# Kernel optimization log

Measured on AMD Instinct MI355X. Metric: run time of the kernel, lower is better.

## Reference

```python
import jax, jax.numpy as jnp
import numpy as np

B, N, D, H = 32, 1024, 512, 8
DH = D // H


def setup_inputs() -> dict:
    key = jax.random.key(0)
    ks = jax.random.split(key, 7)
    s = 1.0 / np.sqrt(D)
    return {
        "x": jax.random.normal(ks[0], (B, N, D), dtype=jnp.float32),
        "Wq": jax.random.uniform(ks[1], (D, D), jnp.float32, -s, s),
        "bq": jax.random.uniform(ks[2], (D,), jnp.float32, -s, s),
        "Wk": jax.random.uniform(ks[3], (D, D), jnp.float32, -s, s),
        "bk": jax.random.uniform(ks[4], (D,), jnp.float32, -s, s),
        "Wv": jax.random.uniform(ks[5], (D, D), jnp.float32, -s, s),
        "bv": jax.random.uniform(ks[6], (D,), jnp.float32, -s, s),
    }


def reference(x, Wq, bq, Wk, bk, Wv, bv):
    # Linear projections (torch Linear: y = x @ W.T + b)
    q = x @ Wq.T + bq
    k = x @ Wk.T + bk
    v = x @ Wv.T + bv
    # Faithful to the original: RAW reshape [B,N,D] -> [B,H,N,D/H] (no transpose!)
    q = q.reshape(B, H, N, DH)
    k = k.reshape(B, H, N, DH)
    v = v.reshape(B, H, N, DH)
    # Scaled dot-product attention
    scores = jnp.einsum("bhnd,bhmd->bhnm", q, k) / jnp.sqrt(jnp.float32(DH))
    attn = jax.nn.softmax(scores, axis=-1)
    y = jnp.einsum("bhnm,bhmd->bhnd", attn, v)
    # Faithful to the original: raw reshape [B,H,N,DH] -> [B,N,H*DH]
    return y.reshape(B, N, H * DH)
```

## Files before the change

kernel.cpp:

```cpp
#include <hip/hip_runtime.h>
#include <hip/hip_bf16.h>
#include <stdint.h>

#define AS_G __attribute__((address_space(1)))
#define AS_L __attribute__((address_space(3)))

typedef short bf16x8 __attribute__((ext_vector_type(8)));
typedef float f32x4  __attribute__((ext_vector_type(4)));
typedef float f32x16 __attribute__((ext_vector_type(16)));
typedef unsigned int u32x2 __attribute__((ext_vector_type(2)));

constexpr int   M_ROWS = 32768;
constexpr float QSCALE = 0.18033688011112042f;

__device__ __forceinline__ ushort f2bf(float f) {
  union { __hip_bfloat16 h; ushort u; } c;
  c.h = __float2bfloat16(f);
  return c.u;
}
__device__ __forceinline__ uint32_t pack2bf(float lo, float hi) {
  union { __hip_bfloat162 b; uint32_t u; } r;
  r.b.x = __float2bfloat16(lo);
  r.b.y = __float2bfloat16(hi);
  return r.u;
}
__device__ __forceinline__ u32x2 pswap(uint32_t x) {
  return __builtin_amdgcn_permlane32_swap(x, x, false, false);
}
__device__ __forceinline__ void gload16(const ushort* g, ushort* l) {
  __builtin_amdgcn_global_load_lds((const AS_G uint32_t*)g, (AS_L uint32_t*)l, 16, 0, 0);
}

__device__ __forceinline__ void cvt8(const float* __restrict__ in,
                                     ushort* __restrict__ out, int i) {
  float4 a = reinterpret_cast<const float4*>(in)[2 * i];
  float4 b = reinterpret_cast<const float4*>(in)[2 * i + 1];
  ushort4 o0 = {f2bf(a.x), f2bf(a.y), f2bf(a.z), f2bf(a.w)};
  ushort4 o1 = {f2bf(b.x), f2bf(b.y), f2bf(b.z), f2bf(b.w)};
  reinterpret_cast<ushort4*>(out)[2 * i]     = o0;
  reinterpret_cast<ushort4*>(out)[2 * i + 1] = o1;
}

__global__ __launch_bounds__(256) void cvt_all_kernel(
    const float* __restrict__ x,  const float* __restrict__ wq,
    const float* __restrict__ wk, const float* __restrict__ wv,
    ushort* __restrict__ xb, ushort* __restrict__ wb) {
  const int b = blockIdx.x, t = threadIdx.x;
  if (b < 2048) {
    const int i0 = b * 256 + t;
#pragma unroll
    for (int rep = 0; rep < 4; ++rep) cvt8(x, xb, i0 + rep * 524288);
  } else {
    const int c = b - 2048, m = c >> 7;
    const float* src = (m == 0) ? wq : (m == 1 ? wk : wv);
    cvt8(src, wb + m * 262144, (c & 127) * 256 + t);
  }
}

__global__ __launch_bounds__(256) void qkv_gemm_kernel(
    const ushort* __restrict__ Xb, const ushort* __restrict__ Wall,
    const float* __restrict__ bq, const float* __restrict__ bk,
    const float* __restrict__ bv,
    ushort* __restrict__ QKV)
{
  __shared__ ushort As[128 * 64];
  __shared__ ushort Bs[128 * 64];

  const int tile = blockIdx.x;
  const int mt  = tile & 255;
  const int cz  = tile >> 8;
  const int mat = cz >> 2;
  const int nt  = cz & 3;

  const ushort* W    = Wall + (size_t)mat * (512 * 512);
  const float*  bias = (mat == 0) ? bq : (mat == 1 ? bk : bv);
  ushort*       Out  = QKV + (size_t)mat * ((size_t)M_ROWS * 512);
  const float   oscale = (mat == 0) ? QSCALE : 1.0f;

  const int m0 = mt * 128, n0 = nt * 128;
  const int t = threadIdx.x, lane = t & 63, wave = t >> 6;
  const int wr = wave >> 1, wc = wave & 1;
  const int l15 = lane & 15, lg = lane >> 4;

  f32x4 acc[4][4];
#pragma unroll
  for (int i = 0; i < 4; i++)
#pragma unroll
    for (int j = 0; j < 4; j++) acc[i][j] = {0.f, 0.f, 0.f, 0.f};

  for (int kt = 0; kt < 8; ++kt) {
    const int k0 = kt * 64;
    __syncthreads();
#pragma unroll
    for (int i = 0; i < 4; ++i) {
      int c = i * 256 + t, row = c >> 3, col8 = (c & 7) * 8;
      gload16(Xb + (size_t)(m0 + row) * 512 + k0 + col8, As + c * 8);
    }
#pragma unroll
    for (int i = 0; i < 4; ++i) {
      int c = i * 256 + t, row = c >> 3, col8 = (c & 7) * 8;
      gload16(W + (size_t)(n0 + row) * 512 + k0 + col8, Bs + c * 8);
    }
    __syncthreads();
#pragma unroll
    for (int ks = 0; ks < 2; ++ks) {
      bf16x8 af[4], bfr[4];
#pragma unroll
      for (int i = 0; i < 4; ++i) {
        af[i]  = *(const bf16x8*)(As + (wr * 64 + i * 16 + l15) * 64 + ks * 32 + lg * 8);
        bfr[i] = *(const bf16x8*)(Bs + (wc * 64 + i * 16 + l15) * 64 + ks * 32 + lg * 8);
      }
#pragma unroll
      for (int i = 0; i < 4; ++i)
#pragma unroll
        for (int j = 0; j < 4; ++j)
          acc[i][j] = __builtin_amdgcn_mfma_f32_16x16x32_bf16(af[i], bfr[j], acc[i][j], 0, 0, 0);
    }
  }
#pragma unroll
  for (int j = 0; j < 4; ++j) {
    const int col = n0 + wc * 64 + j * 16 + l15;
    const float bc = bias[col];
#pragma unroll
    for (int i = 0; i < 4; ++i) {
      const int row0 = m0 + wr * 64 + i * 16 + lg * 4;
#pragma unroll
      for (int r = 0; r < 4; ++r)
        Out[(size_t)(row0 + r) * 512 + col] = f2bf((acc[i][j][r] + bc) * oscale);
    }
  }
}

__global__ __launch_bounds__(256) void vtrans_kernel(
    const ushort* __restrict__ Vn, ushort* __restrict__ VT)
{
  __shared__ ushort T[64][258];
  const int bh = blockIdx.x >> 2, nc = blockIdx.x & 3;
  const ushort* src = Vn + (size_t)bh * 65536 + nc * 16384;
  ushort* dst = VT + (size_t)bh * 65536 + nc * 256;
  const int t = threadIdx.x;
#pragma unroll
  for (int i = 0; i < 8; ++i) {
    int c = i * 256 + t, n = c >> 3, col8 = (c & 7) * 8;
    ushort tmp[8];
    *(int4*)tmp = *(const int4*)(src + n * 64 + col8);
#pragma unroll
    for (int j = 0; j < 8; ++j) T[col8 + j][n] = tmp[j];
  }
  __syncthreads();
#pragma unroll
  for (int i = 0; i < 8; ++i) {
    int c = i * 256 + t, dh = c >> 5, a8 = (c & 31) * 8;
    const int w = a8 & 63;
    const int pbase = (a8 & 192) + (w >> 5) * 32 + ((w >> 4) & 1) * 16
                    + ((w >> 3) & 1) * 4;
    ushort tmp[8];
    *(uint64_t*)(tmp)     = *(const uint64_t*)(&T[dh][pbase]);
    *(uint64_t*)(tmp + 4) = *(const uint64_t*)(&T[dh][pbase + 8]);
    *(int4*)(dst + (size_t)dh * 1024 + a8) = *(const int4*)tmp;
  }
}

__global__ __launch_bounds__(256, 4) void attn_kernel(
    const ushort* __restrict__ QKV,
    const ushort* __restrict__ VTg_,
    float* __restrict__ Out)
{
  constexpr int PLANE = M_ROWS * 512;
  __shared__ ushort SMEM[64 * 258];
  ushort* sK = SMEM;
  ushort* sV = SMEM + 8192;
  float* Lbuf = (float*)SMEM;

  const int raw = blockIdx.x;
  const int blk = ((raw & 7) << 8) | (raw >> 3);
  const int bh = blk >> 3, qb = blk & 7;
  const ushort* Qg  = QKV + (size_t)bh * 65536;
  const ushort* Kg  = QKV + (size_t)PLANE + (size_t)bh * 65536;
  const ushort* Vtg = VTg_ + (size_t)bh * 65536;

  const int t = threadIdx.x, lane = t & 63, wave = t >> 6;
  const int l31 = lane & 31, h = lane >> 5;
  const int q = qb * 128 + wave * 32 + l31;

  bf16x8 qf[4];
#pragma unroll
  for (int ks = 0; ks < 4; ++ks)
    qf[ks] = *(const bf16x8*)(Qg + (size_t)q * 64 + ks * 16 + h * 8);

  float mrow = -1e30f, lrow = 0.f;
  f32x16 o[2];
#pragma unroll
  for (int r = 0; r < 16; ++r) { o[0][r] = 0.f; o[1][r] = 0.f; }

#pragma unroll
  for (int i = 0; i < 2; ++i) {
    int c = i * 256 + t, row = c >> 3, slot = c & 7;
    gload16(Kg + (size_t)row * 64 + ((slot ^ (row & 7)) << 3), sK + c * 8);
    gload16(Vtg + (size_t)row * 1024 + ((slot ^ (row & 7)) << 3), sV + c * 8);
  }
  __syncthreads();

  for (int kv = 0; kv < 16; ++kv) {
    const int cur = kv & 1;
    if (kv < 15) {
      const int nx = cur ^ 1, kn = kv + 1;
#pragma unroll
      for (int i = 0; i < 2; ++i) {
        int c = i * 256 + t, row = c >> 3, slot = c & 7;
        gload16(Kg + (size_t)(kn * 64 + row) * 64 + ((slot ^ (row & 7)) << 3),
                sK + nx * 4096 + c * 8);
        gload16(Vtg + (size_t)row * 1024 + kn * 64 + ((slot ^ (row & 7)) << 3),
                sV + nx * 4096 + c * 8);
      }
    }
    const ushort* Kc = sK + cur * 4096;
    const ushort* Vc = sV + cur * 4096;

    f32x16 st[2];
#pragma unroll
    for (int tt = 0; tt < 2; ++tt) {
      f32x16 a;
#pragma unroll
      for (int r = 0; r < 16; ++r) a[r] = 0.f;
      __builtin_amdgcn_s_setprio(1);
#pragma unroll
      for (int ks = 0; ks < 4; ++ks) {
        const int krow = tt * 32 + l31;
        bf16x8 kf = *(const bf16x8*)(Kc + krow * 64 + (((ks * 2 + h) ^ (krow & 7)) << 3));
        a = __builtin_amdgcn_mfma_f32_32x32x16_bf16(kf, qf[ks], a, 0, 0, 0);
      }
      __builtin_amdgcn_s_setprio(0);
      st[tt] = a;
    }

    float mx;
    {
      float t8[8];
#pragma unroll
      for (int i = 0; i < 8; ++i)
        t8[i] = fmaxf(fmaxf(st[0][i], st[0][i + 8]), fmaxf(st[1][i], st[1][i + 8]));
      float a0 = fmaxf(fmaxf(t8[0], t8[1]), fmaxf(t8[2], t8[3]));
      float a1 = fmaxf(fmaxf(t8[4], t8[5]), fmaxf(t8[6], t8[7]));
      mx = fmaxf(a0, a1);
    }
    {
      u32x2 d = pswap(__float_as_uint(mx));
      mx = fmaxf(__uint_as_float(d.x), __uint_as_float(d.y));
    }
    if (!__all(mx - mrow <= 8.0f)) {
      const float mnew = fmaxf(mrow, mx);
      const float alpha = exp2f(mrow - mnew);
      mrow = mnew;
      lrow *= alpha;
#pragma unroll
      for (int r = 0; r < 16; ++r) { o[0][r] *= alpha; o[1][r] *= alpha; }
    }
#pragma unroll
    for (int tt = 0; tt < 2; ++tt)
#pragma unroll
      for (int r = 0; r < 16; ++r) st[tt][r] = exp2f(st[tt][r] - mrow);
    {
      float s8[8];
#pragma unroll
      for (int i = 0; i < 8; ++i)
        s8[i] = (st[0][i] + st[0][i + 8]) + (st[1][i] + st[1][i + 8]);
      float rs = ((s8[0] + s8[1]) + (s8[2] + s8[3]))
               + ((s8[4] + s8[5]) + (s8[6] + s8[7]));
      u32x2 d = pswap(__float_as_uint(rs));
      lrow += __uint_as_float(d.x) + __uint_as_float(d.y);
    }

#pragma unroll
    for (int tt = 0; tt < 2; ++tt) {
#pragma unroll
      for (int s = 0; s < 2; ++s) {
        union { uint32_t u[4]; bf16x8 v; } pf;
#pragma unroll
        for (int i = 0; i < 4; ++i)
          pf.u[i] = pack2bf(st[tt][8 * s + 2 * i], st[tt][8 * s + 2 * i + 1]);
        const int ks2 = tt * 2 + s;
        __builtin_amdgcn_s_setprio(1);
#pragma unroll
        for (int dt = 0; dt < 2; ++dt) {
          const int drow = dt * 32 + l31;
          bf16x8 vf = *(const bf16x8*)(Vc + drow * 64 +
                                       (((ks2 * 2 + h) ^ (drow & 7)) << 3));
          o[dt] = __builtin_amdgcn_mfma_f32_32x32x16_bf16(vf, pf.v, o[dt], 0, 0, 0);
        }
        __builtin_amdgcn_s_setprio(0);
      }
    }
    __syncthreads();
  }

  const float linv = 1.f / lrow;
#pragma unroll
  for (int dt = 0; dt < 2; ++dt)
#pragma unroll
    for (int r = 0; r < 16; ++r) {
      const int d = dt * 32 + (r & 3) + 8 * (r >> 2) + 4 * h;
      Lbuf[d * 129 + wave * 32 + l31] = o[dt][r] * linv;
    }
  __syncthreads();
  {
    const int qloc = t >> 1, dh = (t & 1) * 32;
    float* ob = Out + (size_t)bh * 65536 + (size_t)(qb * 128 + qloc) * 64 + dh;
#pragma unroll
    for (int c = 0; c < 8; ++c) {
      float4 v = { Lbuf[(dh + 4 * c + 0) * 129 + qloc],
                   Lbuf[(dh + 4 * c + 1) * 129 + qloc],
                   Lbuf[(dh + 4 * c + 2) * 129 + qloc],
                   Lbuf[(dh + 4 * c + 3) * 129 + qloc] };
      *(float4*)(ob + 4 * c) = v;
    }
  }
}

extern "C" void kernel_launch(void* const* d_in, const int* in_sizes, int n_in,
                              void* d_out, int out_size, void* d_ws, size_t ws_size,
                              hipStream_t stream) {
  (void)in_sizes; (void)n_in; (void)out_size; (void)ws_size;
  const float* x  = (const float*)d_in[0];
  const float* Wq = (const float*)d_in[1];
  const float* bq = (const float*)d_in[2];
  const float* Wk = (const float*)d_in[3];
  const float* bk = (const float*)d_in[4];
  const float* Wv = (const float*)d_in[5];
  const float* bv = (const float*)d_in[6];

  ushort* Xb  = (ushort*)d_ws;
  ushort* VT  = (ushort*)d_ws;
  ushort* Wb  = (ushort*)((char*)d_ws + 33554432);
  ushort* QKV = (ushort*)((char*)d_ws + 35127296);
  ushort* Vn  = QKV + 2 * (size_t)M_ROWS * 512;

  cvt_all_kernel<<<2432, 256, 0, stream>>>(x, Wq, Wk, Wv, Xb, Wb);

  qkv_gemm_kernel<<<256 * 12, 256, 0, stream>>>(Xb, Wb, bq, bk, bv, QKV);

  vtrans_kernel<<<1024, 256, 0, stream>>>(Vn, VT);

  attn_kernel<<<256 * 8, 256, 0, stream>>>(QKV, VT, (float*)d_out);
}
```

Measured before the change: 235.6 us.

## Read V directly from global memory and shrink LDS to raise occupancy

Stops staging the transposed V tiles in LDS and has each lane load its V fragments straight from global memory inside the PV MFMA loop. The epilogue transpose buffer is cut to a 32x129 float array, with the output written in two halves, and launch bounds rise from 4 to 6 blocks per SIMD. The aim is to let more workgroups fit per CU and hide latency better, at the cost of uncoalesced per-lane global loads of V in the inner loop, which depend on L2 hits.

After: 529.1 us. 2.25x slower.

```diff
diff --git a/kernel.cpp b/kernel.cpp
--- a/kernel.cpp
+++ b/kernel.cpp
@@ -161,16 +161,14 @@
   }
 }
 
-__global__ __launch_bounds__(256, 4) void attn_kernel(
+__global__ __launch_bounds__(256, 6) void attn_kernel(
     const ushort* __restrict__ QKV,
     const ushort* __restrict__ VTg_,
     float* __restrict__ Out)
 {
   constexpr int PLANE = M_ROWS * 512;
-  __shared__ ushort SMEM[64 * 258];
-  ushort* sK = SMEM;
-  ushort* sV = SMEM + 8192;
-  float* Lbuf = (float*)SMEM;
+  __shared__ float Lbuf[32 * 129];
+  ushort* sK = (ushort*)Lbuf;
 
   const int raw = blockIdx.x;
   const int blk = ((raw & 7) << 8) | (raw >> 3);
@@ -197,7 +195,6 @@
   for (int i = 0; i < 2; ++i) {
     int c = i * 256 + t, row = c >> 3, slot = c & 7;
     gload16(Kg + (size_t)row * 64 + ((slot ^ (row & 7)) << 3), sK + c * 8);
-    gload16(Vtg + (size_t)row * 1024 + ((slot ^ (row & 7)) << 3), sV + c * 8);
   }
   __syncthreads();
 
@@ -210,12 +207,10 @@
         int c = i * 256 + t, row = c >> 3, slot = c & 7;
         gload16(Kg + (size_t)(kn * 64 + row) * 64 + ((slot ^ (row & 7)) << 3),
                 sK + nx * 4096 + c * 8);
-        gload16(Vtg + (size_t)row * 1024 + kn * 64 + ((slot ^ (row & 7)) << 3),
-                sV + nx * 4096 + c * 8);
       }
     }
-    const ushort* Kc = sK + cur * 4096;
-    const ushort* Vc = sV + cur * 4096;
+    const ushort* Kc  = sK + cur * 4096;
+    const ushort* Vkv = Vtg + kv * 64;
 
     f32x16 st[2];
 #pragma unroll
@@ -284,8 +279,7 @@
 #pragma unroll
         for (int dt = 0; dt < 2; ++dt) {
           const int drow = dt * 32 + l31;
-          bf16x8 vf = *(const bf16x8*)(Vc + drow * 64 +
-                                       (((ks2 * 2 + h) ^ (drow & 7)) << 3));
+          bf16x8 vf = *(const bf16x8*)(Vkv + (size_t)drow * 1024 + ks2 * 16 + h * 8);
           o[dt] = __builtin_amdgcn_mfma_f32_32x32x16_bf16(vf, pf.v, o[dt], 0, 0, 0);
         }
         __builtin_amdgcn_s_setprio(0);
@@ -296,22 +290,23 @@
 
   const float linv = 1.f / lrow;
 #pragma unroll
-  for (int dt = 0; dt < 2; ++dt)
+  for (int half = 0; half < 2; ++half) {
+    __syncthreads();
 #pragma unroll
     for (int r = 0; r < 16; ++r) {
-      const int d = dt * 32 + (r & 3) + 8 * (r >> 2) + 4 * h;
-      Lbuf[d * 129 + wave * 32 + l31] = o[dt][r] * linv;
-    }
-  __syncthreads();
-  {
-    const int qloc = t >> 1, dh = (t & 1) * 32;
-    float* ob = Out + (size_t)bh * 65536 + (size_t)(qb * 128 + qloc) * 64 + dh;
-#pragma unroll
-    for (int c = 0; c < 8; ++c) {
-      float4 v = { Lbuf[(dh + 4 * c + 0) * 129 + qloc],
-                   Lbuf[(dh + 4 * c + 1) * 129 + qloc],
-                   Lbuf[(dh + 4 * c + 2) * 129 + qloc],
-                   Lbuf[(dh + 4 * c + 3) * 129 + qloc] };
+      const int dloc = (r & 3) + 8 * (r >> 2) + 4 * h;
+      Lbuf[dloc * 129 + wave * 32 + l31] = o[half][r] * linv;
+    }
+    __syncthreads();
+    const int qloc = t >> 1, ds0 = (t & 1) * 16;
+    float* ob = Out + (size_t)bh * 65536 + (size_t)(qb * 128 + qloc) * 64
+              + half * 32 + ds0;
+#pragma unroll
+    for (int c = 0; c < 4; ++c) {
+      float4 v = { Lbuf[(ds0 + 4 * c + 0) * 129 + qloc],
+                   Lbuf[(ds0 + 4 * c + 1) * 129 + qloc],
+                   Lbuf[(ds0 + 4 * c + 2) * 129 + qloc],
+                   Lbuf[(ds0 + 4 * c + 3) * 129 + qloc] };
       *(float4*)(ob + 4 * c) = v;
     }
   }
```
